# Kernel optimization log

Hardware: AMD Instinct MI355X
Metric: run time of the kernel (lower is better)

## Reference

```python
import jax, jax.numpy as jnp
import numpy as np

N0, N1, N2, N3, N4 = 50000, 100000, 20000, 20000, 20000
E0, E1, E01 = 800000, 1600000, 200000
C = 64
SLOPE = 0.2


def _xavier(k, shape):
    fan_in, fan_out = shape[0], shape[-1]
    lim = float(np.sqrt(6.0 / (fan_in + fan_out)))
    return jax.random.uniform(k, shape, minval=-lim, maxval=lim, dtype=jnp.float32)


def setup_inputs() -> dict:
    key = jax.random.key(0)
    ks = jax.random.split(key, 16)
    return {
        "x_0": jax.random.normal(ks[0], (N0, C), jnp.float32),
        "x_1": jax.random.normal(ks[1], (N1, C), jnp.float32),
        "x_2": jax.random.normal(ks[2], (N2, C), jnp.float32),
        "x_3": jax.random.normal(ks[3], (N3, C), jnp.float32),
        "x_4": jax.random.normal(ks[4], (N4, C), jnp.float32),
        # sparse adjacency_0 [N0,N0], adjacency_1 [N1,N1] as COO (row=i target, col=j source), values=1
        "adj0_idx": jax.random.randint(ks[5], (2, E0), 0, N0, dtype=jnp.int32),
        "adj1_idx": jax.random.randint(ks[6], (2, E1), 0, N1, dtype=jnp.int32),
        # sparse incidence_0_1 [N0,N1]: row = 0-cell (target), col = 1-cell (source)
        "inc01_t": jax.random.randint(ks[7], (E01,), 0, N0, dtype=jnp.int32),
        "inc01_s": jax.random.randint(ks[8], (E01,), 0, N1, dtype=jnp.int32),
        # HBS_0 params
        "W0": _xavier(ks[9], (C, C)),
        "a0": _xavier(ks[10], (2 * C, 1))[:, 0],
        # HBS_1 params
        "W1": _xavier(ks[11], (C, C)),
        "a1": _xavier(ks[12], (2 * C, 1))[:, 0],
        # HBNS params (source = x_1, target = x_0)
        "Ws": _xavier(ks[13], (C, C)),
        "Wt": _xavier(ks[14], (C, C)),
        "a_ns": _xavier(ks[15], (2 * C, 1))[:, 0],
    }


def _row_norm(vals, rows, n_rows):
    # sparse row-sum normalization (softmax_attention=False path)
    rs = jax.ops.segment_sum(vals, rows, num_segments=n_rows)
    denom = jnp.where(rs == 0, 1.0, rs)
    return vals / denom[rows]


def _hbs(x, idx, W, a, n):
    # Higher-order attention Block for Squared neighborhoods, m_hop=1.
    m = x @ W                               # [n, C]
    i, j = idx[0], idx[1]                   # edge (i <- j)
    # score_ij = leaky_relu(cat(m_i, m_j) @ a) computed without materializing [E, 2C]
    p_l = m @ a[:C]                         # [n]
    p_r = m @ a[C:]                         # [n]
    e = jax.nn.leaky_relu(p_l[i] + p_r[j], SLOPE)   # [E]
    att = _row_norm(e, i, n)                # [E]
    # (att .* A) @ m  with binary A values
    return jax.ops.segment_sum(att[:, None] * m[j], i, num_segments=n)


def _hbns(x_s, x_t, t_idx, s_idx, Ws, Wt, a, n_s, n_t):
    # Higher-order attention Block for Non-Squared neighborhoods.
    sm = x_s @ Ws                           # [n_s, C] messages from source cells
    tm = x_t @ Wt                           # [n_t, C] messages from target cells
    p_s = sm @ a[:C]                        # [n_s]
    p_t = tm @ a[C:]                        # [n_t]
    e = jax.nn.leaky_relu(p_s[s_idx] + p_t[t_idx], SLOPE)   # [E01]
    att_s_to_t = _row_norm(e, t_idx, n_t)   # normalize per target row
    att_t_to_s = _row_norm(e, s_idx, n_s)   # normalize per source row (transposed)
    msg_on_target = jax.ops.segment_sum(att_s_to_t[:, None] * sm[s_idx], t_idx, num_segments=n_t)
    msg_on_source = jax.ops.segment_sum(att_t_to_s[:, None] * tm[t_idx], s_idx, num_segments=n_s)
    return msg_on_source, msg_on_target    # (x_0_to_1, x_1_to_0)


def reference(x_0, x_1, x_2, x_3, x_4, adj0_idx, adj1_idx, inc01_t, inc01_s,
              W0, a0, W1, a1, Ws, Wt, a_ns):
    x_0_to_0 = _hbs(x_0, adj0_idx, W0, a0, N0)
    x_1_to_1 = _hbs(x_1, adj1_idx, W1, a1, N1)
    x_0_to_1, x_1_to_0 = _hbns(x_1, x_0, inc01_t, inc01_s, Ws, Wt, a_ns, N1, N0)
    # Aggregation(aggr_func='sum', update_func=None)
    x_0_level1 = x_0_to_0 + x_1_to_0
    x_1_level1 = x_1_to_1 + x_0_to_1
    return (x_0_level1, x_1_level1, x_2, x_3, x_4)
```

## Files before the change

kernel.cpp:

```cpp
#include <hip/hip_runtime.h>

#define CDIM 64
#define SLOPE 0.2f
#define PART_EDGES 8192
#define BW 128

__device__ __forceinline__ float lrelu(float v) { return v > 0.f ? v : SLOPE * v; }

__device__ __forceinline__ void gemm_tile(const float* __restrict__ X,
                                          const float* __restrict__ Wa, float* __restrict__ Ya,
                                          const float* __restrict__ Wb, float* __restrict__ Yb,
                                          int n, int tile,
                                          float* sX, float* sWaT, float* sWbT)
{
    const int tid = threadIdx.x;
    const int lane = tid & 63;
    const int q = tid >> 6;

    for (int idx = tid; idx < 4096; idx += 256) {
        int k = idx >> 6, c = idx & 63;
        sWaT[c * 66 + k] = Wa[idx];
        sWbT[c * 66 + k] = Wb[idx];
    }
    const int rowbase = tile << 6;
#pragma unroll
    for (int i = 0; i < 4; ++i) {
        int f = tid + i * 256;
        int r = f >> 4, k4 = f & 15;
        int row = rowbase + r;
        float4 v = make_float4(0.f, 0.f, 0.f, 0.f);
        if (row < n) v = *reinterpret_cast<const float4*>(X + (size_t)row * 64 + k4 * 4);
        *reinterpret_cast<float4*>(&sX[r * 68 + k4 * 4]) = v;
    }
    __syncthreads();

    const int r0 = q * 16;
    float accA[16], accB[16];
#pragma unroll
    for (int r = 0; r < 16; ++r) { accA[r] = 0.f; accB[r] = 0.f; }

    for (int k4 = 0; k4 < 16; ++k4) {
        const float2 wa0 = *reinterpret_cast<const float2*>(&sWaT[lane * 66 + k4 * 4]);
        const float2 wa1 = *reinterpret_cast<const float2*>(&sWaT[lane * 66 + k4 * 4 + 2]);
        const float2 wb0 = *reinterpret_cast<const float2*>(&sWbT[lane * 66 + k4 * 4]);
        const float2 wb1 = *reinterpret_cast<const float2*>(&sWbT[lane * 66 + k4 * 4 + 2]);
#pragma unroll
        for (int r = 0; r < 16; ++r) {
            const float4 xv = *reinterpret_cast<const float4*>(&sX[(r0 + r) * 68 + k4 * 4]);
            accA[r] = fmaf(xv.x, wa0.x, accA[r]);
            accA[r] = fmaf(xv.y, wa0.y, accA[r]);
            accA[r] = fmaf(xv.z, wa1.x, accA[r]);
            accA[r] = fmaf(xv.w, wa1.y, accA[r]);
            accB[r] = fmaf(xv.x, wb0.x, accB[r]);
            accB[r] = fmaf(xv.y, wb0.y, accB[r]);
            accB[r] = fmaf(xv.z, wb1.x, accB[r]);
            accB[r] = fmaf(xv.w, wb1.y, accB[r]);
        }
    }
#pragma unroll
    for (int r = 0; r < 16; ++r) {
        int row = rowbase + r0 + r;
        if (row < n) {
            Ya[(size_t)row * 64 + lane] = accA[r];
            Yb[(size_t)row * 64 + lane] = accB[r];
        }
    }
}

__global__ void gemm_pair_kernel(const float* __restrict__ X0,
                                 const float* __restrict__ W0, float* __restrict__ m0,
                                 const float* __restrict__ Wt, float* __restrict__ tm,
                                 int n0, int t0,
                                 const float* __restrict__ X1,
                                 const float* __restrict__ W1, float* __restrict__ m1,
                                 const float* __restrict__ Ws, float* __restrict__ sm,
                                 int n1)
{
    __shared__ float sX[64 * 68];
    __shared__ float sWaT[64 * 66];
    __shared__ float sWbT[64 * 66];
    int b = blockIdx.x;
    if (b < t0) gemm_tile(X0, W0, m0, Wt, tm, n0, b, sX, sWaT, sWbT);
    else        gemm_tile(X1, W1, m1, Ws, sm, n1, b - t0, sX, sWaT, sWbT);
}

__global__ void ppass_kernel(const float* __restrict__ m0, const float* __restrict__ m1,
                             const float* __restrict__ sm, const float* __restrict__ tm,
                             const float* __restrict__ a0, const float* __restrict__ a1,
                             const float* __restrict__ ans,
                             float* __restrict__ pl0, float* __restrict__ pr0,
                             float* __restrict__ pl1, float* __restrict__ pr1,
                             float* __restrict__ pls, float* __restrict__ prs,
                             float* __restrict__ plt, float* __restrict__ prt,
                             int N0, int N1)
{
    int g = blockIdx.x * blockDim.x + threadIdx.x;
    if (g >= 2 * (N0 + N1)) return;
    const float* M; const float* a; float* pL; float* pR; int r;
    if (g < N0)                { M = m0; a = a0;  pL = pl0; pR = pr0; r = g; }
    else if (g < N0 + N1)      { M = m1; a = a1;  pL = pl1; pR = pr1; r = g - N0; }
    else if (g < N0 + 2 * N1)  { M = sm; a = ans; pL = pls; pR = prs; r = g - N0 - N1; }
    else                       { M = tm; a = ans; pL = plt; pR = prt; r = g - N0 - 2 * N1; }

    const float4* row = reinterpret_cast<const float4*>(M + (size_t)r * 64);
    float sl = 0.f, sr = 0.f;
#pragma unroll
    for (int k4 = 0; k4 < 16; ++k4) {
        float4 xv = row[k4];
        float4 al = *reinterpret_cast<const float4*>(a + k4 * 4);
        float4 ar = *reinterpret_cast<const float4*>(a + 64 + k4 * 4);
        sl = fmaf(xv.x, al.x, sl); sl = fmaf(xv.y, al.y, sl);
        sl = fmaf(xv.z, al.z, sl); sl = fmaf(xv.w, al.w, sl);
        sr = fmaf(xv.x, ar.x, sr); sr = fmaf(xv.y, ar.y, sr);
        sr = fmaf(xv.z, ar.z, sr); sr = fmaf(xv.w, ar.w, sr);
    }
    pL[r] = sl;
    pR[r] = sr;
}

struct PartDesc {
    const int* keys[4];
    const int* vals[4];
    int E[4];
    int nb[4];
    int bcap[4];
    int bufbase[4];
    int pblk[5];
};

__global__ void partition_kernel(PartDesc d, int2* __restrict__ gbuf, int* __restrict__ bcur)
{
    __shared__ int hist[1024];
    __shared__ int sbase[1024];
    int b = blockIdx.x;
    int l = (b >= d.pblk[2]) ? ((b >= d.pblk[3]) ? 3 : 2) : ((b >= d.pblk[1]) ? 1 : 0);
    const int start = (b - d.pblk[l]) * PART_EDGES;
    const int E = d.E[l];
    const int nb = d.nb[l];
    const int t = threadIdx.x;
    for (int i = t; i < nb; i += 256) hist[i] = 0;
    __syncthreads();
    const int* kp = d.keys[l];
    const int* vp = d.vals[l];

#pragma unroll
    for (int seg = 0; seg < 8; ++seg) {
        int i4 = start + seg * 1024 + t * 4;
        if (i4 + 3 < E) {
            int4 k4 = *reinterpret_cast<const int4*>(kp + i4);
            atomicAdd(&hist[k4.x >> 7], 1);
            atomicAdd(&hist[k4.y >> 7], 1);
            atomicAdd(&hist[k4.z >> 7], 1);
            atomicAdd(&hist[k4.w >> 7], 1);
        } else {
            int e4 = min(i4 + 4, E);
            for (int u = i4; u < e4; ++u) atomicAdd(&hist[kp[u] >> 7], 1);
        }
    }
    __syncthreads();
    for (int i = t; i < nb; i += 256) {
        int c = hist[i];
        sbase[i] = c ? atomicAdd(&bcur[l * 1024 + i], c) : 0;
    }
    __syncthreads();
    for (int i = t; i < nb; i += 256) hist[i] = 0;
    __syncthreads();

    const int bcap = d.bcap[l];
    int2* buf = gbuf + d.bufbase[l];
#pragma unroll
    for (int seg = 0; seg < 8; ++seg) {
        int i4 = start + seg * 1024 + t * 4;
        if (i4 + 3 < E) {
            int4 k4 = *reinterpret_cast<const int4*>(kp + i4);
            int4 v4 = *reinterpret_cast<const int4*>(vp + i4);
            int ks[4] = { k4.x, k4.y, k4.z, k4.w };
            int vs[4] = { v4.x, v4.y, v4.z, v4.w };
#pragma unroll
            for (int e = 0; e < 4; ++e) {
                int bk = ks[e] >> 7;
                int r = atomicAdd(&hist[bk], 1);
                int slot = sbase[bk] + r;
                if (slot < bcap) buf[(size_t)bk * bcap + slot] = make_int2(ks[e], vs[e]);
            }
        } else {
            int e4 = min(i4 + 4, E);
            for (int u = i4; u < e4; ++u) {
                int k = kp[u];
                int bk = k >> 7;
                int r = atomicAdd(&hist[bk], 1);
                int slot = sbase[bk] + r;
                if (slot < bcap) buf[(size_t)bk * bcap + slot] = make_int2(k, vp[u]);
            }
        }
    }
}

struct GB {
    const int2* bufA; const int* curA; int bcapA;
    const float* MA; const float* plA; const float* prA;
    const int2* bufB; const int* curB; int bcapB;
    const float* MB; const float* plB; const float* prB;
    float* out; int n;
};

__device__ __forceinline__ void gatherrow_lds(const int* __restrict__ sorted, int s0, int deg,
                                              const float* __restrict__ M,
                                              const float* __restrict__ pr,
                                              float pl, int gg, int c4,
                                              float4& acc, double& se)
{
    for (int p = 0; p < deg; p += 8) {
        int i1 = p + gg;
        int i2 = p + 4 + gg;
        bool ok1 = i1 < deg;
        bool ok2 = i2 < deg;
        int j1 = ok1 ? sorted[s0 + i1] : 0;
        int j2 = ok2 ? sorted[s0 + i2] : 0;
        float e1 = ok1 ? lrelu(pl + pr[j1]) : 0.f;
        float e2 = ok2 ? lrelu(pl + pr[j2]) : 0.f;
        const float4 r1 = *reinterpret_cast<const float4*>(M + (size_t)j1 * 64 + c4);
        const float4 r2 = *reinterpret_cast<const float4*>(M + (size_t)j2 * 64 + c4);
        se += (double)e1 + (double)e2;
        acc.x = fmaf(e1, r1.x, fmaf(e2, r2.x, acc.x));
        acc.y = fmaf(e1, r1.y, fmaf(e2, r2.y, acc.y));
        acc.z = fmaf(e1, r1.z, fmaf(e2, r2.z, acc.z));
        acc.w = fmaf(e1, r1.w, fmaf(e2, r2.w, acc.w));
    }
}

__global__ __launch_bounds__(512) void gatherbkt_kernel(GB ga, GB gb, int nbSplit)
{
    __shared__ int countsA[BW], startsA[BW], cursA[BW];
    __shared__ int countsB[BW], startsB[BW], cursB[BW];
    __shared__ int sortedA[2560];
    __shared__ int sortedB[768];

    const bool first = blockIdx.x < nbSplit;
    GB g = first ? ga : gb;
    const int bucket = first ? blockIdx.x : (blockIdx.x - nbSplit);
    const int lo = bucket * BW;
    const int t = threadIdx.x;

    if (t < BW) { countsA[t] = 0; countsB[t] = 0; }
    __syncthreads();

    const int cntA = min(g.curA[bucket], g.bcapA);
    const int cntB = min(g.curB[bucket], g.bcapB);
    const int2* bufA = g.bufA + (size_t)bucket * g.bcapA;
    const int2* bufB = g.bufB + (size_t)bucket * g.bcapB;

    for (int i = t; i < cntA; i += 512) atomicAdd(&countsA[bufA[i].x - lo], 1);
    for (int i = t; i < cntB; i += 512) atomicAdd(&countsB[bufB[i].x - lo], 1);
    __syncthreads();

    {
        int idx = t & (BW - 1);
        bool a = t < BW;
        bool b = (t >= BW) && (t < 2 * BW);
        if (a) startsA[idx] = countsA[idx];
        if (b) startsB[idx] = countsB[idx];
        __syncthreads();
        for (int off = 1; off < BW; off <<= 1) {
            int vA = (a && idx >= off) ? startsA[idx - off] : 0;
            int vB = (b && idx >= off) ? startsB[idx - off] : 0;
            __syncthreads();
            if (a) startsA[idx] += vA;
            if (b) startsB[idx] += vB;
            __syncthreads();
        }
        if (a) { startsA[idx] -= countsA[idx]; cursA[idx] = startsA[idx]; }
        if (b) { startsB[idx] -= countsB[idx]; cursB[idx] = startsB[idx]; }
    }
    __syncthreads();
    for (int i = t; i < cntA; i += 512) {
        int2 kv = bufA[i];
        sortedA[atomicAdd(&cursA[kv.x - lo], 1)] = kv.y;
    }
    for (int i = t; i < cntB; i += 512) {
        int2 kv = bufB[i];
        sortedB[atomicAdd(&cursB[kv.x - lo], 1)] = kv.y;
    }
    __syncthreads();

    const int lane = t & 63;
    const int wid = t >> 6;
    const int gg = lane >> 4;
    const int c4 = (lane & 15) << 2;

    for (int rr = wid; rr < BW; rr += 8) {
        int row = lo + rr;
        if (row >= g.n) break;
        float4 accA = make_float4(0.f, 0.f, 0.f, 0.f);
        float4 accB = make_float4(0.f, 0.f, 0.f, 0.f);
        double seA = 0.0, seB = 0.0;

        gatherrow_lds(sortedA, startsA[rr], countsA[rr], g.MA, g.prA, g.plA[row], gg, c4, accA, seA);
        gatherrow_lds(sortedB, startsB[rr], countsB[rr], g.MB, g.prB, g.plB[row], gg, c4, accB, seB);

        seA += __shfl_xor(seA, 16, 64); seA += __shfl_xor(seA, 32, 64);
        seB += __shfl_xor(seB, 16, 64); seB += __shfl_xor(seB, 32, 64);
        float rA = (float)(1.0 / ((seA == 0.0) ? 1.0 : seA));
        float rB = (float)(1.0 / ((seB == 0.0) ? 1.0 : seB));

        float4 part;
        part.x = accA.x * rA + accB.x * rB;
        part.y = accA.y * rA + accB.y * rB;
        part.z = accA.z * rA + accB.z * rB;
        part.w = accA.w * rA + accB.w * rB;
        part.x += __shfl_xor(part.x, 16, 64); part.x += __shfl_xor(part.x, 32, 64);
        part.y += __shfl_xor(part.y, 16, 64); part.y += __shfl_xor(part.y, 32, 64);
        part.z += __shfl_xor(part.z, 16, 64); part.z += __shfl_xor(part.z, 32, 64);
        part.w += __shfl_xor(part.w, 16, 64); part.w += __shfl_xor(part.w, 32, 64);

        if (gg == 0) *reinterpret_cast<float4*>(g.out + (size_t)row * 64 + c4) = part;
    }
}

__global__ void copy3_kernel(const float4* __restrict__ s0, const float4* __restrict__ s1,
                             const float4* __restrict__ s2, float4* __restrict__ dst, int n4)
{
    int i = blockIdx.x * blockDim.x + threadIdx.x;
    if (i < n4)            dst[i] = s0[i];
    else if (i < 2 * n4)   dst[i] = s1[i - n4];
    else if (i < 3 * n4)   dst[i] = s2[i - 2 * n4];
}

extern "C" void kernel_launch(void* const* d_in, const int* in_sizes, int n_in,
                              void* d_out, int out_size, void* d_ws, size_t ws_size,
                              hipStream_t stream)
{
    const float* x0  = (const float*)d_in[0];
    const float* x1  = (const float*)d_in[1];
    const float* x2  = (const float*)d_in[2];
    const float* x3  = (const float*)d_in[3];
    const float* x4  = (const float*)d_in[4];
    const int*   adj0 = (const int*)d_in[5];
    const int*   adj1 = (const int*)d_in[6];
    const int*   inct = (const int*)d_in[7];
    const int*   incs = (const int*)d_in[8];
    const float* W0  = (const float*)d_in[9];
    const float* a0  = (const float*)d_in[10];
    const float* W1  = (const float*)d_in[11];
    const float* a1  = (const float*)d_in[12];
    const float* Ws  = (const float*)d_in[13];
    const float* Wt  = (const float*)d_in[14];
    const float* ans = (const float*)d_in[15];

    const int N0  = in_sizes[0] / CDIM;
    const int N1  = in_sizes[1] / CDIM;
    const int NP  = in_sizes[2];
    const int E0  = in_sizes[5] / 2;
    const int E1  = in_sizes[6] / 2;
    const int E01 = in_sizes[7];

    float* out0 = (float*)d_out;
    float* out1 = out0 + (size_t)N0 * CDIM;
    float* outp = out1 + (size_t)N1 * CDIM;

    char* w = (char*)d_ws;
    size_t off = 0;
    float* m0  = (float*)(w + off); off += (size_t)N0 * CDIM * 4;
    float* m1  = (float*)(w + off); off += (size_t)N1 * CDIM * 4;
    float* sm  = (float*)(w + off); off += (size_t)N1 * CDIM * 4;
    float* tm  = (float*)(w + off); off += (size_t)N0 * CDIM * 4;
    float* pl0 = (float*)(w + off); off += (size_t)N0 * 4;
    float* pr0 = (float*)(w + off); off += (size_t)N0 * 4;
    float* pl1 = (float*)(w + off); off += (size_t)N1 * 4;
    float* pr1 = (float*)(w + off); off += (size_t)N1 * 4;
    float* pls = (float*)(w + off); off += (size_t)N1 * 4;
    float* prs = (float*)(w + off); off += (size_t)N1 * 4;
    float* plt = (float*)(w + off); off += (size_t)N0 * 4;
    float* prt = (float*)(w + off); off += (size_t)N0 * 4;
    int* bcur = (int*)(w + off); off += 4096 * 4;
    const int nb0 = (N0 + BW - 1) / BW;
    const int nb1 = (N1 + BW - 1) / BW;
    const int BC0 = 2560, BC1 = 2560, BCT = 768, BCS = 512;
    int2* gbuf = (int2*)(w + off);
    (void)ws_size; (void)n_in; (void)out_size;

    dim3 blk(256);

    PartDesc d;
    d.keys[0] = adj0; d.vals[0] = adj0 + E0; d.E[0] = E0;  d.nb[0] = nb0; d.bcap[0] = BC0;
    d.keys[1] = adj1; d.vals[1] = adj1 + E1; d.E[1] = E1;  d.nb[1] = nb1; d.bcap[1] = BC1;
    d.keys[2] = inct; d.vals[2] = incs;      d.E[2] = E01; d.nb[2] = nb0; d.bcap[2] = BCT;
    d.keys[3] = incs; d.vals[3] = inct;      d.E[3] = E01; d.nb[3] = nb1; d.bcap[3] = BCS;
    d.bufbase[0] = 0;
    d.bufbase[1] = d.bufbase[0] + nb0 * BC0;
    d.bufbase[2] = d.bufbase[1] + nb1 * BC1;
    d.bufbase[3] = d.bufbase[2] + nb0 * BCT;
    d.pblk[0] = 0;
    for (int l = 0; l < 4; ++l) d.pblk[l + 1] = d.pblk[l] + (d.E[l] + PART_EDGES - 1) / PART_EDGES;

    hipMemsetAsync(bcur, 0, 4096 * 4, stream);
    partition_kernel<<<d.pblk[4], blk, 0, stream>>>(d, gbuf, bcur);

    const int t0 = (N0 + 63) / 64, t1 = (N1 + 63) / 64;
    gemm_pair_kernel<<<t0 + t1, blk, 0, stream>>>(x0, W0, m0, Wt, tm, N0, t0,
                                                  x1, W1, m1, Ws, sm, N1);
    ppass_kernel<<<(2 * (N0 + N1) + 255) / 256, blk, 0, stream>>>(
        m0, m1, sm, tm, a0, a1, ans,
        pl0, pr0, pl1, pr1, pls, prs, plt, prt, N0, N1);

    GB gb0 = { gbuf + d.bufbase[0], bcur + 0 * 1024, BC0, m0, pl0, pr0,
               gbuf + d.bufbase[2], bcur + 2 * 1024, BCT, sm, prt, pls,
               out0, N0 };
    GB gb1 = { gbuf + d.bufbase[1], bcur + 1 * 1024, BC1, m1, pl1, pr1,
               gbuf + d.bufbase[3], bcur + 3 * 1024, BCS, tm, pls, prt,
               out1, N1 };
    gatherbkt_kernel<<<nb0 + nb1, 512, 0, stream>>>(gb0, gb1, nb0);

    int n4 = NP / 4;
    copy3_kernel<<<(3 * n4 + 255) / 256, blk, 0, stream>>>(
        (const float4*)x2, (const float4*)x3, (const float4*)x4, (float4*)outp, n4);
}
```

Baseline: 291.8 us.

## Fuse partition, GEMM, attention projections and passthrough copy into one front kernel

```diff
diff --git a/kernel.cpp b/kernel.cpp
--- a/kernel.cpp
+++ b/kernel.cpp
@@ -6,117 +6,6 @@
 #define BW 128
 
 __device__ __forceinline__ float lrelu(float v) { return v > 0.f ? v : SLOPE * v; }
-
-__device__ __forceinline__ void gemm_tile(const float* __restrict__ X,
-                                          const float* __restrict__ Wa, float* __restrict__ Ya,
-                                          const float* __restrict__ Wb, float* __restrict__ Yb,
-                                          int n, int tile,
-                                          float* sX, float* sWaT, float* sWbT)
-{
-    const int tid = threadIdx.x;
-    const int lane = tid & 63;
-    const int q = tid >> 6;
-
-    for (int idx = tid; idx < 4096; idx += 256) {
-        int k = idx >> 6, c = idx & 63;
-        sWaT[c * 66 + k] = Wa[idx];
-        sWbT[c * 66 + k] = Wb[idx];
-    }
-    const int rowbase = tile << 6;
-#pragma unroll
-    for (int i = 0; i < 4; ++i) {
-        int f = tid + i * 256;
-        int r = f >> 4, k4 = f & 15;
-        int row = rowbase + r;
-        float4 v = make_float4(0.f, 0.f, 0.f, 0.f);
-        if (row < n) v = *reinterpret_cast<const float4*>(X + (size_t)row * 64 + k4 * 4);
-        *reinterpret_cast<float4*>(&sX[r * 68 + k4 * 4]) = v;
-    }
-    __syncthreads();
-
-    const int r0 = q * 16;
-    float accA[16], accB[16];
-#pragma unroll
-    for (int r = 0; r < 16; ++r) { accA[r] = 0.f; accB[r] = 0.f; }
-
-    for (int k4 = 0; k4 < 16; ++k4) {
-        const float2 wa0 = *reinterpret_cast<const float2*>(&sWaT[lane * 66 + k4 * 4]);
-        const float2 wa1 = *reinterpret_cast<const float2*>(&sWaT[lane * 66 + k4 * 4 + 2]);
-        const float2 wb0 = *reinterpret_cast<const float2*>(&sWbT[lane * 66 + k4 * 4]);
-        const float2 wb1 = *reinterpret_cast<const float2*>(&sWbT[lane * 66 + k4 * 4 + 2]);
-#pragma unroll
-        for (int r = 0; r < 16; ++r) {
-            const float4 xv = *reinterpret_cast<const float4*>(&sX[(r0 + r) * 68 + k4 * 4]);
-            accA[r] = fmaf(xv.x, wa0.x, accA[r]);
-            accA[r] = fmaf(xv.y, wa0.y, accA[r]);
-            accA[r] = fmaf(xv.z, wa1.x, accA[r]);
-            accA[r] = fmaf(xv.w, wa1.y, accA[r]);
-            accB[r] = fmaf(xv.x, wb0.x, accB[r]);
-            accB[r] = fmaf(xv.y, wb0.y, accB[r]);
-            accB[r] = fmaf(xv.z, wb1.x, accB[r]);
-            accB[r] = fmaf(xv.w, wb1.y, accB[r]);
-        }
-    }
-#pragma unroll
-    for (int r = 0; r < 16; ++r) {
-        int row = rowbase + r0 + r;
-        if (row < n) {
-            Ya[(size_t)row * 64 + lane] = accA[r];
-            Yb[(size_t)row * 64 + lane] = accB[r];
-        }
-    }
-}
-
-__global__ void gemm_pair_kernel(const float* __restrict__ X0,
-                                 const float* __restrict__ W0, float* __restrict__ m0,
-                                 const float* __restrict__ Wt, float* __restrict__ tm,
-                                 int n0, int t0,
-                                 const float* __restrict__ X1,
-                                 const float* __restrict__ W1, float* __restrict__ m1,
-                                 const float* __restrict__ Ws, float* __restrict__ sm,
-                                 int n1)
-{
-    __shared__ float sX[64 * 68];
-    __shared__ float sWaT[64 * 66];
-    __shared__ float sWbT[64 * 66];
-    int b = blockIdx.x;
-    if (b < t0) gemm_tile(X0, W0, m0, Wt, tm, n0, b, sX, sWaT, sWbT);
-    else        gemm_tile(X1, W1, m1, Ws, sm, n1, b - t0, sX, sWaT, sWbT);
-}
-
-__global__ void ppass_kernel(const float* __restrict__ m0, const float* __restrict__ m1,
-                             const float* __restrict__ sm, const float* __restrict__ tm,
-                             const float* __restrict__ a0, const float* __restrict__ a1,
-                             const float* __restrict__ ans,
-                             float* __restrict__ pl0, float* __restrict__ pr0,
-                             float* __restrict__ pl1, float* __restrict__ pr1,
-                             float* __restrict__ pls, float* __restrict__ prs,
-                             float* __restrict__ plt, float* __restrict__ prt,
-                             int N0, int N1)
-{
-    int g = blockIdx.x * blockDim.x + threadIdx.x;
-    if (g >= 2 * (N0 + N1)) return;
-    const float* M; const float* a; float* pL; float* pR; int r;
-    if (g < N0)                { M = m0; a = a0;  pL = pl0; pR = pr0; r = g; }
-    else if (g < N0 + N1)      { M = m1; a = a1;  pL = pl1; pR = pr1; r = g - N0; }
-    else if (g < N0 + 2 * N1)  { M = sm; a = ans; pL = pls; pR = prs; r = g - N0 - N1; }
-    else                       { M = tm; a = ans; pL = plt; pR = prt; r = g - N0 - 2 * N1; }
-
-    const float4* row = reinterpret_cast<const float4*>(M + (size_t)r * 64);
-    float sl = 0.f, sr = 0.f;
-#pragma unroll
-    for (int k4 = 0; k4 < 16; ++k4) {
-        float4 xv = row[k4];
-        float4 al = *reinterpret_cast<const float4*>(a + k4 * 4);
-        float4 ar = *reinterpret_cast<const float4*>(a + 64 + k4 * 4);
-        sl = fmaf(xv.x, al.x, sl); sl = fmaf(xv.y, al.y, sl);
-        sl = fmaf(xv.z, al.z, sl); sl = fmaf(xv.w, al.w, sl);
-        sr = fmaf(xv.x, ar.x, sr); sr = fmaf(xv.y, ar.y, sr);
-        sr = fmaf(xv.z, ar.z, sr); sr = fmaf(xv.w, ar.w, sr);
-    }
-    pL[r] = sl;
-    pR[r] = sr;
-}
 
 struct PartDesc {
     const int* keys[4];
@@ -128,11 +17,22 @@
     int pblk[5];
 };
 
-__global__ void partition_kernel(PartDesc d, int2* __restrict__ gbuf, int* __restrict__ bcur)
-{
-    __shared__ int hist[1024];
-    __shared__ int sbase[1024];
-    int b = blockIdx.x;
+struct FrontDesc {
+    PartDesc pd;
+    const float *X0, *W0, *Wt, *a0;
+    float *m0, *tm, *pl0, *pr0, *plt, *prt;
+    int n0, t0;
+    const float *X1, *W1, *Ws, *a1, *ans;
+    float *m1, *sm, *pl1, *pr1, *pls, *prs;
+    int n1, t1;
+    const float4 *c0, *c1, *c2;
+    float4* dst;
+    int n4;
+};
+
+__device__ void partition_body(const PartDesc& d, int b, int2* __restrict__ gbuf,
+                               int* __restrict__ bcur, int* hist, int* sbase)
+{
     int l = (b >= d.pblk[2]) ? ((b >= d.pblk[3]) ? 3 : 2) : ((b >= d.pblk[1]) ? 1 : 0);
     const int start = (b - d.pblk[l]) * PART_EDGES;
     const int E = d.E[l];
@@ -194,6 +94,154 @@
             }
         }
     }
+}
+
+__device__ void gemm_tile_p(const float* __restrict__ X,
+                            const float* __restrict__ Wa, float* __restrict__ Ya,
+                            const float* __restrict__ aa, float* __restrict__ pLa, float* __restrict__ pRa,
+                            const float* __restrict__ Wb, float* __restrict__ Yb,
+                            const float* __restrict__ ab, float* __restrict__ pLb, float* __restrict__ pRb,
+                            int n, int tile,
+                            float* sX, float* sWaT, float* sWbT, float* sa2)
+{
+    const int tid = threadIdx.x;
+    const int lane = tid & 63;
+    const int q = tid >> 6;
+
+    for (int idx = tid; idx < 4096; idx += 256) {
+        int k = idx >> 6, c = idx & 63;
+        sWaT[c * 66 + k] = Wa[idx];
+        sWbT[c * 66 + k] = Wb[idx];
+    }
+    if (tid < 128) sa2[tid] = aa[tid];
+    else sa2[tid] = ab[tid - 128];
+
+    const int rowbase = tile << 6;
+#pragma unroll
+    for (int i = 0; i < 4; ++i) {
+        int f = tid + i * 256;
+        int r = f >> 4, k4 = f & 15;
+        int row = rowbase + r;
+        float4 v = make_float4(0.f, 0.f, 0.f, 0.f);
+        if (row < n) v = *reinterpret_cast<const float4*>(X + (size_t)row * 64 + k4 * 4);
+        *reinterpret_cast<float4*>(&sX[r * 68 + k4 * 4]) = v;
+    }
+    __syncthreads();
+
+    const int r0 = q * 16;
+    float accA[16], accB[16];
+#pragma unroll
+    for (int r = 0; r < 16; ++r) { accA[r] = 0.f; accB[r] = 0.f; }
+
+    for (int k4 = 0; k4 < 16; ++k4) {
+        const float2 wa0 = *reinterpret_cast<const float2*>(&sWaT[lane * 66 + k4 * 4]);
+        const float2 wa1 = *reinterpret_cast<const float2*>(&sWaT[lane * 66 + k4 * 4 + 2]);
+        const float2 wb0 = *reinterpret_cast<const float2*>(&sWbT[lane * 66 + k4 * 4]);
+        const float2 wb1 = *reinterpret_cast<const float2*>(&sWbT[lane * 66 + k4 * 4 + 2]);
+#pragma unroll
+        for (int r = 0; r < 16; ++r) {
+            const float4 xv = *reinterpret_cast<const float4*>(&sX[(r0 + r) * 68 + k4 * 4]);
+            accA[r] = fmaf(xv.x, wa0.x, accA[r]);
+            accA[r] = fmaf(xv.y, wa0.y, accA[r]);
+            accA[r] = fmaf(xv.z, wa1.x, accA[r]);
+            accA[r] = fmaf(xv.w, wa1.y, accA[r]);
+            accB[r] = fmaf(xv.x, wb0.x, accB[r]);
+            accB[r] = fmaf(xv.y, wb0.y, accB[r]);
+            accB[r] = fmaf(xv.z, wb1.x, accB[r]);
+            accB[r] = fmaf(xv.w, wb1.y, accB[r]);
+        }
+    }
+#pragma unroll
+    for (int r = 0; r < 16; ++r) {
+        int row = rowbase + r0 + r;
+        if (row < n) {
+            Ya[(size_t)row * 64 + lane] = accA[r];
+            Yb[(size_t)row * 64 + lane] = accB[r];
+        }
+    }
+
+    __syncthreads();
+#pragma unroll
+    for (int r = 0; r < 16; ++r) sX[(r0 + r) * 68 + lane] = accA[r];
+    __syncthreads();
+    if (tid < 64) {
+        int row = rowbase + tid;
+        if (row < n) {
+            const float4* rp = reinterpret_cast<const float4*>(&sX[tid * 68]);
+            float sl = 0.f, sr = 0.f;
+#pragma unroll
+            for (int k4 = 0; k4 < 16; ++k4) {
+                float4 xv = rp[k4];
+                float4 al = *reinterpret_cast<const float4*>(&sa2[k4 * 4]);
+                float4 ar = *reinterpret_cast<const float4*>(&sa2[64 + k4 * 4]);
+                sl = fmaf(xv.x, al.x, sl); sl = fmaf(xv.y, al.y, sl);
+                sl = fmaf(xv.z, al.z, sl); sl = fmaf(xv.w, al.w, sl);
+                sr = fmaf(xv.x, ar.x, sr); sr = fmaf(xv.y, ar.y, sr);
+                sr = fmaf(xv.z, ar.z, sr); sr = fmaf(xv.w, ar.w, sr);
+            }
+            pLa[row] = sl;
+            pRa[row] = sr;
+        }
+    }
+    __syncthreads();
+#pragma unroll
+    for (int r = 0; r < 16; ++r) sX[(r0 + r) * 68 + lane] = accB[r];
+    __syncthreads();
+    if (tid < 64) {
+        int row = rowbase + tid;
+        if (row < n) {
+            const float4* rp = reinterpret_cast<const float4*>(&sX[tid * 68]);
+            float sl = 0.f, sr = 0.f;
+#pragma unroll
+            for (int k4 = 0; k4 < 16; ++k4) {
+                float4 xv = rp[k4];
+                float4 al = *reinterpret_cast<const float4*>(&sa2[128 + k4 * 4]);
+                float4 ar = *reinterpret_cast<const float4*>(&sa2[192 + k4 * 4]);
+                sl = fmaf(xv.x, al.x, sl); sl = fmaf(xv.y, al.y, sl);
+                sl = fmaf(xv.z, al.z, sl); sl = fmaf(xv.w, al.w, sl);
+                sr = fmaf(xv.x, ar.x, sr); sr = fmaf(xv.y, ar.y, sr);
+                sr = fmaf(xv.z, ar.z, sr); sr = fmaf(xv.w, ar.w, sr);
+            }
+            pLb[row] = sl;
+            pRb[row] = sr;
+        }
+    }
+}
+
+__global__ __launch_bounds__(256) void front_kernel(FrontDesc fd, int2* __restrict__ gbuf,
+                                                    int* __restrict__ bcur)
+{
+    __shared__ float sX[64 * 68];
+    __shared__ float sWaT[64 * 66];
+    __shared__ float sWbT[64 * 66];
+    __shared__ float sa2[256];
+
+    int b = blockIdx.x;
+    const int nPart = fd.pd.pblk[4];
+    if (b < nPart) {
+        partition_body(fd.pd, b, gbuf, bcur, (int*)sX, ((int*)sX) + 1024);
+        return;
+    }
+    b -= nPart;
+    if (b < fd.t0) {
+        gemm_tile_p(fd.X0, fd.W0, fd.m0, fd.a0, fd.pl0, fd.pr0,
+                    fd.Wt, fd.tm, fd.ans, fd.plt, fd.prt,
+                    fd.n0, b, sX, sWaT, sWbT, sa2);
+        return;
+    }
+    b -= fd.t0;
+    if (b < fd.t1) {
+        gemm_tile_p(fd.X1, fd.W1, fd.m1, fd.a1, fd.pl1, fd.pr1,
+                    fd.Ws, fd.sm, fd.ans, fd.pls, fd.prs,
+                    fd.n1, b, sX, sWaT, sWbT, sa2);
+        return;
+    }
+    b -= fd.t1;
+    int i = b * 256 + threadIdx.x;
+    int n4 = fd.n4;
+    if (i < n4)            fd.dst[i] = fd.c0[i];
+    else if (i < 2 * n4)   fd.dst[i] = fd.c1[i - n4];
+    else if (i < 3 * n4)   fd.dst[i] = fd.c2[i - 2 * n4];
 }
 
 struct GB {
@@ -315,15 +363,6 @@
 
         if (gg == 0) *reinterpret_cast<float4*>(g.out + (size_t)row * 64 + c4) = part;
     }
-}
-
-__global__ void copy3_kernel(const float4* __restrict__ s0, const float4* __restrict__ s1,
-                             const float4* __restrict__ s2, float4* __restrict__ dst, int n4)
-{
-    int i = blockIdx.x * blockDim.x + threadIdx.x;
-    if (i < n4)            dst[i] = s0[i];
-    else if (i < 2 * n4)   dst[i] = s1[i - n4];
-    else if (i < 3 * n4)   dst[i] = s2[i - 2 * n4];
 }
 
 extern "C" void kernel_launch(void* const* d_in, const int* in_sizes, int n_in,
@@ -379,9 +418,8 @@
     int2* gbuf = (int2*)(w + off);
     (void)ws_size; (void)n_in; (void)out_size;
 
-    dim3 blk(256);
-
-    PartDesc d;
+    FrontDesc fd;
+    PartDesc& d = fd.pd;
     d.keys[0] = adj0; d.vals[0] = adj0 + E0; d.E[0] = E0;  d.nb[0] = nb0; d.bcap[0] = BC0;
     d.keys[1] = adj1; d.vals[1] = adj1 + E1; d.E[1] = E1;  d.nb[1] = nb1; d.bcap[1] = BC1;
     d.keys[2] = inct; d.vals[2] = incs;      d.E[2] = E01; d.nb[2] = nb0; d.bcap[2] = BCT;
@@ -393,15 +431,20 @@
     d.pblk[0] = 0;
     for (int l = 0; l < 4; ++l) d.pblk[l + 1] = d.pblk[l] + (d.E[l] + PART_EDGES - 1) / PART_EDGES;
 
+    fd.X0 = x0; fd.W0 = W0; fd.Wt = Wt; fd.a0 = a0;
+    fd.m0 = m0; fd.tm = tm; fd.pl0 = pl0; fd.pr0 = pr0; fd.plt = plt; fd.prt = prt;
+    fd.n0 = N0; fd.t0 = (N0 + 63) / 64;
+    fd.X1 = x1; fd.W1 = W1; fd.Ws = Ws; fd.a1 = a1; fd.ans = ans;
+    fd.m1 = m1; fd.sm = sm; fd.pl1 = pl1; fd.pr1 = pr1; fd.pls = pls; fd.prs = prs;
+    fd.n1 = N1; fd.t1 = (N1 + 63) / 64;
+    fd.c0 = (const float4*)x2; fd.c1 = (const float4*)x3; fd.c2 = (const float4*)x4;
+    fd.dst = (float4*)outp; fd.n4 = NP / 4;
+
+    const int nCopyBlk = (3 * fd.n4 + 255) / 256;
+    const int nFront = d.pblk[4] + fd.t0 + fd.t1 + nCopyBlk;
+
     hipMemsetAsync(bcur, 0, 4096 * 4, stream);
-    partition_kernel<<<d.pblk[4], blk, 0, stream>>>(d, gbuf, bcur);
-
-    const int t0 = (N0 + 63) / 64, t1 = (N1 + 63) / 64;
-    gemm_pair_kernel<<<t0 + t1, blk, 0, stream>>>(x0, W0, m0, Wt, tm, N0, t0,
-                                                  x1, W1, m1, Ws, sm, N1);
-    ppass_kernel<<<(2 * (N0 + N1) + 255) / 256, blk, 0, stream>>>(
-        m0, m1, sm, tm, a0, a1, ans,
-        pl0, pr0, pl1, pr1, pls, prs, plt, prt, N0, N1);
+    front_kernel<<<nFront, 256, 0, stream>>>(fd, gbuf, bcur);
 
     GB gb0 = { gbuf + d.bufbase[0], bcur + 0 * 1024, BC0, m0, pl0, pr0,
                gbuf + d.bufbase[2], bcur + 2 * 1024, BCT, sm, prt, pls,
@@ -410,8 +453,4 @@
                gbuf + d.bufbase[3], bcur + 3 * 1024, BCS, tm, pls, prt,
                out1, N1 };
     gatherbkt_kernel<<<nb0 + nb1, 512, 0, stream>>>(gb0, gb1, nb0);
-
-    int n4 = NP / 4;
-    copy3_kernel<<<(3 * n4 + 255) / 256, blk, 0, stream>>>(
-        (const float4*)x2, (const float4*)x3, (const float4*)x4, (float4*)outp, n4);
-}
+}
```

After: 255.6 us. 12.4% less time.
